# Performance work log

Measured on AMD Instinct MI355X. Metric: run time of the kernel, lower is better.

The kernel has to match this reference:

```python
import jax, jax.numpy as jnp
import numpy as np

N_NODES = 50000
N_EDGES = 640000
D = 128
OUT = 1


def setup_inputs() -> dict:
    key = jax.random.key(0)
    k1, k2, k3, k4 = jax.random.split(key, 4)
    X = jax.random.normal(k1, (N_NODES, D), dtype=jnp.float32)
    edge_index = jax.random.randint(k2, (2, N_EDGES), 0, N_NODES, dtype=jnp.int64)
    W1 = jax.random.normal(k3, (OUT, D), dtype=jnp.float32) / np.sqrt(D)
    W2 = jax.random.normal(k4, (OUT, D), dtype=jnp.float32) / np.sqrt(D)
    return {"X": X, "edge_index": edge_index, "W1": W1, "W2": W2}


def reference(X, edge_index, W1, W2):
    # E[e] = W1 @ X[src[e]] + W2 @ X[dst[e]]
    # Gather endpoint features then apply the two bias-free linears and add.
    src, dst = edge_index[0], edge_index[1]
    Xs = X[src]                      # [E, D]
    Xd = X[dst]                      # [E, D]
    return jnp.einsum('ed,od->eo', Xs, W1) + jnp.einsum('ed,od->eo', Xd, W2)  # [E, OUT]
```

## Files before the change

### kernel.cpp

```cpp
#include <hip/hip_runtime.h>

#define N_NODES 50000
#define N_EDGES 640000
#define D 128

__global__ __launch_bounds__(256) void node_scores_kernel(
    const float* __restrict__ X,
    const float* __restrict__ W1,
    const float* __restrict__ W2,
    float* __restrict__ s1,
    float* __restrict__ s2,
    int n_nodes, int total_groups)
{
    const int lane = threadIdx.x & 63;
    const int sl   = lane & 15;
    const int sub  = lane >> 4;
    const int wave = blockIdx.x * (blockDim.x >> 6) + (threadIdx.x >> 6);
    const int g    = wave * 4 + sub;

    const float4* W1v = (const float4*)W1;
    const float4* W2v = (const float4*)W2;
    const float4 w1a = W1v[sl * 2],     w1b = W1v[sl * 2 + 1];
    const float4 w2a = W2v[sl * 2],     w2b = W2v[sl * 2 + 1];

    for (int n = g; n < n_nodes; n += total_groups) {
        const float4* Xv = (const float4*)(X + (size_t)n * D);
        const float4 x0 = Xv[sl * 2];
        const float4 x1 = Xv[sl * 2 + 1];
        float p1 = x0.x * w1a.x + x0.y * w1a.y + x0.z * w1a.z + x0.w * w1a.w
                 + x1.x * w1b.x + x1.y * w1b.y + x1.z * w1b.z + x1.w * w1b.w;
        float p2 = x0.x * w2a.x + x0.y * w2a.y + x0.z * w2a.z + x0.w * w2a.w
                 + x1.x * w2b.x + x1.y * w2b.y + x1.z * w2b.z + x1.w * w2b.w;
        #pragma unroll
        for (int off = 8; off > 0; off >>= 1) {
            p1 += __shfl_xor(p1, off, 64);
            p2 += __shfl_xor(p2, off, 64);
        }
        if (sl == 0) {
            s1[n] = p1;
            s2[n] = p2;
        }
    }
}

__global__ __launch_bounds__(256) void edge_combine_kernel(
    const int* __restrict__ src,
    const int* __restrict__ dst,
    const float* __restrict__ s1,
    const float* __restrict__ s2,
    float* __restrict__ out,
    int n8)
{
    const int i = blockIdx.x * blockDim.x + threadIdx.x;
    if (i < n8) {
        const int4 sa = ((const int4*)src)[2 * i];
        const int4 sb = ((const int4*)src)[2 * i + 1];
        const int4 da = ((const int4*)dst)[2 * i];
        const int4 db = ((const int4*)dst)[2 * i + 1];
        float4 oa, ob;
        oa.x = s1[sa.x] + s2[da.x];
        oa.y = s1[sa.y] + s2[da.y];
        oa.z = s1[sa.z] + s2[da.z];
        oa.w = s1[sa.w] + s2[da.w];
        ob.x = s1[sb.x] + s2[db.x];
        ob.y = s1[sb.y] + s2[db.y];
        ob.z = s1[sb.z] + s2[db.z];
        ob.w = s1[sb.w] + s2[db.w];
        ((float4*)out)[2 * i]     = oa;
        ((float4*)out)[2 * i + 1] = ob;
    }
}

extern "C" void kernel_launch(void* const* d_in, const int* in_sizes, int n_in,
                              void* d_out, int out_size, void* d_ws, size_t ws_size,
                              hipStream_t stream) {
    const float* X  = (const float*)d_in[0];
    const int*   ei = (const int*)d_in[1];
    const float* W1 = (const float*)d_in[2];
    const float* W2 = (const float*)d_in[3];
    float* out = (float*)d_out;

    float* s1 = (float*)d_ws;
    float* s2 = s1 + N_NODES;

    const int blocks1 = 512;
    node_scores_kernel<<<blocks1, 256, 0, stream>>>(X, W1, W2, s1, s2,
                                                    N_NODES, blocks1 * 16);

    const int n8 = N_EDGES / 8;
    edge_combine_kernel<<<(n8 + 255) / 256, 256, 0, stream>>>(
        ei, ei + N_EDGES, s1, s2, out, n8);
}
```

Measured before the change: 84.36 us.

## Fuse node-score and edge-combine kernels into one cooperative kernel with grid sync

Merges the two launches into a single cooperative kernel that computes per-node scores, does a grid-wide barrier, then runs a grid-stride loop over edges to gather and add the scores. The aim is to drop the second launch and the gap between kernels. Loads of X and the edge indices, and the output stores, now use nontemporal hints. The grid shrinks to 256 blocks, so each thread does more work, and the grid sync plus cooperative-launch overhead may offset what is saved.

```diff
diff --git a/kernel.cpp b/kernel.cpp
--- a/kernel.cpp
+++ b/kernel.cpp
@@ -1,32 +1,40 @@
 #include <hip/hip_runtime.h>
+#include <hip/hip_cooperative_groups.h>
+
+namespace cg = cooperative_groups;
 
 #define N_NODES 50000
 #define N_EDGES 640000
 #define D 128
 
-__global__ __launch_bounds__(256) void node_scores_kernel(
+typedef float f4 __attribute__((ext_vector_type(4)));
+typedef int   i4 __attribute__((ext_vector_type(4)));
+
+__global__ __launch_bounds__(256) void fused_edge_decoder_kernel(
     const float* __restrict__ X,
+    const int* __restrict__ src,
+    const int* __restrict__ dst,
     const float* __restrict__ W1,
     const float* __restrict__ W2,
     float* __restrict__ s1,
     float* __restrict__ s2,
-    int n_nodes, int total_groups)
+    float* __restrict__ out)
 {
     const int lane = threadIdx.x & 63;
     const int sl   = lane & 15;
-    const int sub  = lane >> 4;
-    const int wave = blockIdx.x * (blockDim.x >> 6) + (threadIdx.x >> 6);
-    const int g    = wave * 4 + sub;
+    const int wave = blockIdx.x * 4 + (threadIdx.x >> 6);
+    const int g    = wave * 4 + (lane >> 4);
+    const int total_groups = gridDim.x * 16;
 
-    const float4* W1v = (const float4*)W1;
-    const float4* W2v = (const float4*)W2;
-    const float4 w1a = W1v[sl * 2],     w1b = W1v[sl * 2 + 1];
-    const float4 w2a = W2v[sl * 2],     w2b = W2v[sl * 2 + 1];
+    const f4* W1v = (const f4*)W1;
+    const f4* W2v = (const f4*)W2;
+    const f4 w1a = W1v[sl * 2], w1b = W1v[sl * 2 + 1];
+    const f4 w2a = W2v[sl * 2], w2b = W2v[sl * 2 + 1];
 
-    for (int n = g; n < n_nodes; n += total_groups) {
-        const float4* Xv = (const float4*)(X + (size_t)n * D);
-        const float4 x0 = Xv[sl * 2];
-        const float4 x1 = Xv[sl * 2 + 1];
+    for (int n = g; n < N_NODES; n += total_groups) {
+        const f4* Xv = (const f4*)(X + (size_t)n * D);
+        const f4 x0 = __builtin_nontemporal_load(Xv + sl * 2);
+        const f4 x1 = __builtin_nontemporal_load(Xv + sl * 2 + 1);
         float p1 = x0.x * w1a.x + x0.y * w1a.y + x0.z * w1a.z + x0.w * w1a.w
                  + x1.x * w1b.x + x1.y * w1b.y + x1.z * w1b.z + x1.w * w1b.w;
         float p2 = x0.x * w2a.x + x0.y * w2a.y + x0.z * w2a.z + x0.w * w2a.w
@@ -41,23 +49,17 @@
             s2[n] = p2;
         }
     }
-}
 
-__global__ __launch_bounds__(256) void edge_combine_kernel(
-    const int* __restrict__ src,
-    const int* __restrict__ dst,
-    const float* __restrict__ s1,
-    const float* __restrict__ s2,
-    float* __restrict__ out,
-    int n8)
-{
-    const int i = blockIdx.x * blockDim.x + threadIdx.x;
-    if (i < n8) {
-        const int4 sa = ((const int4*)src)[2 * i];
-        const int4 sb = ((const int4*)src)[2 * i + 1];
-        const int4 da = ((const int4*)dst)[2 * i];
-        const int4 db = ((const int4*)dst)[2 * i + 1];
-        float4 oa, ob;
+    cg::this_grid().sync();
+
+    const int n8 = N_EDGES / 8;
+    const int nthreads = gridDim.x * blockDim.x;
+    for (int i = blockIdx.x * blockDim.x + threadIdx.x; i < n8; i += nthreads) {
+        const i4 sa = __builtin_nontemporal_load((const i4*)src + 2 * i);
+        const i4 sb = __builtin_nontemporal_load((const i4*)src + 2 * i + 1);
+        const i4 da = __builtin_nontemporal_load((const i4*)dst + 2 * i);
+        const i4 db = __builtin_nontemporal_load((const i4*)dst + 2 * i + 1);
+        f4 oa, ob;
         oa.x = s1[sa.x] + s2[da.x];
         oa.y = s1[sa.y] + s2[da.y];
         oa.z = s1[sa.z] + s2[da.z];
@@ -66,8 +68,8 @@
         ob.y = s1[sb.y] + s2[db.y];
         ob.z = s1[sb.z] + s2[db.z];
         ob.w = s1[sb.w] + s2[db.w];
-        ((float4*)out)[2 * i]     = oa;
-        ((float4*)out)[2 * i + 1] = ob;
+        __builtin_nontemporal_store(oa, (f4*)out + 2 * i);
+        __builtin_nontemporal_store(ob, (f4*)out + 2 * i + 1);
     }
 }
 
@@ -83,11 +85,11 @@
     float* s1 = (float*)d_ws;
     float* s2 = s1 + N_NODES;
 
-    const int blocks1 = 512;
-    node_scores_kernel<<<blocks1, 256, 0, stream>>>(X, W1, W2, s1, s2,
-                                                    N_NODES, blocks1 * 16);
+    const int* src = ei;
+    const int* dst = ei + N_EDGES;
 
-    const int n8 = N_EDGES / 8;
-    edge_combine_kernel<<<(n8 + 255) / 256, 256, 0, stream>>>(
-        ei, ei + N_EDGES, s1, s2, out, n8);
+    void* args[] = {(void*)&X, (void*)&src, (void*)&dst, (void*)&W1,
+                    (void*)&W2, (void*)&s1, (void*)&s2, (void*)&out};
+    hipLaunchCooperativeKernel((const void*)fused_edge_decoder_kernel,
+                               dim3(256), dim3(256), args, 0, stream);
 }
```

Result: slower. 134.3 us (+59.2%).
